# Performance work log

Hardware: AMD Instinct MI355X
Metric: run time of the kernel (lower is better)

The kernel has to match this reference:

```python
import jax, jax.numpy as jnp
import numpy as np

B, S, D, H = 2, 2048, 1024, 16
HD = D // H  # head_dim = 64

def setup_inputs() -> dict:
    key = jax.random.key(0)
    ks = jax.random.split(key, 12)
    sc = 0.02
    return {
        "x": jax.random.normal(ks[0], (B, S, D), dtype=jnp.float32),
        "docking_scores": jax.random.uniform(ks[1], (B, S), dtype=jnp.float32),
        # weights stored as (in, out): y = x @ W + b (equivalent to torch Linear with W=weight.T)
        "Wq": jax.random.normal(ks[2], (D, D), dtype=jnp.float32) * sc,
        "bq": jnp.zeros((D,), dtype=jnp.float32),
        "Wk": jax.random.normal(ks[3], (D, D), dtype=jnp.float32) * sc,
        "bk": jnp.zeros((D,), dtype=jnp.float32),
        "Wv": jax.random.normal(ks[4], (D, D), dtype=jnp.float32) * sc,
        "bv": jnp.zeros((D,), dtype=jnp.float32),
        "Wo": jax.random.normal(ks[5], (D, D), dtype=jnp.float32) * sc,
        "bo": jnp.zeros((D,), dtype=jnp.float32),
        "beta": jnp.asarray(0.5, dtype=jnp.float32),
    }

def reference(x, docking_scores, Wq, bq, Wk, bk, Wv, bv, Wo, bo, beta):
    b, s, d = x.shape
    # project and split heads: (B, H, S, HD)
    def heads(y):
        return y.reshape(b, s, H, HD).transpose(0, 2, 1, 3)
    Q = heads(x @ Wq + bq)
    K = heads(x @ Wk + bk)
    V = heads(x @ Wv + bv)
    # full attention scores (B, H, S, S) — materialized as in the source
    scores = jnp.einsum('bhqd,bhkd->bhqk', Q, K) / np.float32(np.sqrt(HD))
    attn = jax.nn.softmax(scores, axis=-1)
    # docking blend: daa_type != ALL -> blend with per-key docking scores
    ds = docking_scores[:, None, None, :]  # (B, 1, 1, S)
    attn = (1.0 - beta) * attn + beta * ds
    ctx = jnp.einsum('bhqk,bhkd->bhqd', attn, V)
    ctx = ctx.transpose(0, 2, 1, 3).reshape(b, s, d)
    return ctx @ Wo + bo
```

## Files before the change

### kernel.cpp

```cpp
#include <hip/hip_runtime.h>

typedef __attribute__((ext_vector_type(8))) short short8;
typedef __attribute__((ext_vector_type(4))) short short4v;
typedef __attribute__((ext_vector_type(4))) float f32x4;

__device__ __forceinline__ short f2bf(float f) {
  unsigned u = __builtin_bit_cast(unsigned, f);
  u += 0x7fffu + ((u >> 16) & 1u);
  return (short)(u >> 16);
}
__device__ __forceinline__ float bf2f(short s) {
  unsigned u = ((unsigned)(unsigned short)s) << 16;
  return __builtin_bit_cast(float, u);
}
__device__ __forceinline__ void async_load16(const short* g, short* l) {
  __builtin_amdgcn_global_load_lds(
      (const __attribute__((address_space(1))) unsigned int*)g,
      (__attribute__((address_space(3))) unsigned int*)l, 16, 0, 0);
}

__global__ __launch_bounds__(256) void convert_x(const float* __restrict__ x,
                                                 short* __restrict__ xb) {
  int i = (blockIdx.x * 256 + threadIdx.x) * 4;
  float4 v = *(const float4*)(x + i);
  short4v o;
  o[0] = f2bf(v.x); o[1] = f2bf(v.y); o[2] = f2bf(v.z); o[3] = f2bf(v.w);
  *(short4v*)(xb + i) = o;
}

__global__ __launch_bounds__(256) void transpose_w(
    const float* __restrict__ W0, const float* __restrict__ W1,
    const float* __restrict__ W2, const float* __restrict__ W3,
    short* __restrict__ T0, short* __restrict__ T1,
    short* __restrict__ T2, short* __restrict__ T3) {
  const float* W; short* T;
  switch (blockIdx.z) {
    case 0: W = W0; T = T0; break;
    case 1: W = W1; T = T1; break;
    case 2: W = W2; T = T2; break;
    default: W = W3; T = T3; break;
  }
  __shared__ float tile[32][33];
  int tx = threadIdx.x & 31, ty = threadIdx.x >> 5;
  int c = blockIdx.x * 32 + tx;
  #pragma unroll
  for (int i = 0; i < 4; ++i) {
    int r = blockIdx.y * 32 + ty + i * 8;
    tile[ty + i * 8][tx] = W[(size_t)r * 1024 + c];
  }
  __syncthreads();
  int k = blockIdx.y * 32 + tx;
  #pragma unroll
  for (int i = 0; i < 4; ++i) {
    int n = blockIdx.x * 32 + ty + i * 8;
    T[(size_t)n * 1024 + k] = f2bf(tile[tx][ty + i * 8]);
  }
}

__device__ __forceinline__ void gemm_core_128(
    const short* __restrict__ A, const short* __restrict__ Bt,
    int m0, int n0, short* As, short* Bs, f32x4 acc[4][4]) {
  const int tid = threadIdx.x;
  const int wave = tid >> 6, lane = tid & 63;
  const int wm = wave >> 1, wn = wave & 1;
  const int lr = lane & 15, quad = lane >> 4;
  for (int k0 = 0; k0 < 1024; k0 += 32) {
    __syncthreads();
    #pragma unroll
    for (int c2 = 0; c2 < 2; ++c2) {
      int c = wave * 2 + c2;
      int row = c * 16 + (lane >> 2);
      int cbp = lane & 3;
      int sw = (cbp ^ ((row >> 1) & 3)) << 3;
      async_load16(A + (size_t)(m0 + row) * 1024 + k0 + sw, As + c * 512);
      async_load16(Bt + (size_t)(n0 + row) * 1024 + k0 + sw, Bs + c * 512);
    }
    __syncthreads();
    short8 af[4], bf[4];
    #pragma unroll
    for (int i = 0; i < 4; ++i) {
      int ra = wm * 64 + i * 16 + lr;
      af[i] = *(const short8*)(As + ra * 32 + ((quad ^ ((ra >> 1) & 3)) << 3));
      int rb = wn * 64 + i * 16 + lr;
      bf[i] = *(const short8*)(Bs + rb * 32 + ((quad ^ ((rb >> 1) & 3)) << 3));
    }
    #pragma unroll
    for (int i = 0; i < 4; ++i)
      #pragma unroll
      for (int j = 0; j < 4; ++j)
        acc[i][j] = __builtin_amdgcn_mfma_f32_16x16x32_bf16(af[i], bf[j], acc[i][j], 0, 0, 0);
  }
}

__global__ __launch_bounds__(256, 2) void qkv_gemm(
    const short* __restrict__ xb,
    const short* __restrict__ WqT, const short* __restrict__ WkT, const short* __restrict__ WvT,
    const float* __restrict__ bq, const float* __restrict__ bk, const float* __restrict__ bv,
    short* __restrict__ Qb, short* __restrict__ Kb, short* __restrict__ Vt) {
  __shared__ short As[128 * 32];
  __shared__ short Bs[128 * 32];
  int which = blockIdx.x >> 3;
  int n0 = (blockIdx.x & 7) * 128;
  int m0 = blockIdx.y * 128;
  const short* Bt = (which == 0) ? WqT : (which == 1) ? WkT : WvT;
  const float* bias = (which == 0) ? bq : (which == 1) ? bk : bv;
  f32x4 acc[4][4] = {};
  gemm_core_128(xb, Bt, m0, n0, As, Bs, acc);
  const int lane = threadIdx.x & 63, wave = threadIdx.x >> 6;
  const int wm = wave >> 1, wn = wave & 1;
  const int lr = lane & 15, quad = lane >> 4;
  if (which < 2) {
    short* Out = (which == 0) ? Qb : Kb;
    #pragma unroll
    for (int i = 0; i < 4; ++i)
      #pragma unroll
      for (int j = 0; j < 4; ++j) {
        int col = n0 + wn * 64 + j * 16 + lr;
        float bb = bias[col];
        int rowb = m0 + wm * 64 + i * 16 + quad * 4;
        #pragma unroll
        for (int r = 0; r < 4; ++r)
          Out[(size_t)(rowb + r) * 1024 + col] = f2bf(acc[i][j][r] + bb);
      }
  } else {
    #pragma unroll
    for (int i = 0; i < 4; ++i)
      #pragma unroll
      for (int j = 0; j < 4; ++j) {
        int col = n0 + wn * 64 + j * 16 + lr;
        float bb = bias[col];
        int h = col >> 6, d = col & 63;
        int rowb = m0 + wm * 64 + i * 16 + quad * 4;
        int b = rowb >> 11, s = rowb & 2047;
        short4v pk;
        #pragma unroll
        for (int r = 0; r < 4; ++r) pk[r] = f2bf(acc[i][j][r] + bb);
        *(short4v*)(Vt + ((size_t)(b * 16 + h) * 64 + d) * 2048 + s) = pk;
      }
  }
}

__global__ __launch_bounds__(256) void dsv_kernel(const short* __restrict__ Vt,
                                                  const float* __restrict__ ds,
                                                  float* __restrict__ dsV) {
  int bh = blockIdx.x;
  int b = bh >> 4;
  int tid = threadIdx.x;
  int d = tid >> 2, part = tid & 3;
  const short* vrow = Vt + ((size_t)bh * 64 + d) * 2048 + part * 512;
  const float* dsrow = ds + (size_t)b * 2048 + part * 512;
  float acc = 0.f;
  for (int i = 0; i < 512; i += 8) {
    short8 v = *(const short8*)(vrow + i);
    float4 f0 = *(const float4*)(dsrow + i);
    float4 f1 = *(const float4*)(dsrow + i + 4);
    acc += f0.x * bf2f(v[0]) + f0.y * bf2f(v[1]) + f0.z * bf2f(v[2]) + f0.w * bf2f(v[3]);
    acc += f1.x * bf2f(v[4]) + f1.y * bf2f(v[5]) + f1.z * bf2f(v[6]) + f1.w * bf2f(v[7]);
  }
  acc += __shfl_xor(acc, 1);
  acc += __shfl_xor(acc, 2);
  if (part == 0) dsV[bh * 64 + d] = acc;
}

__global__ __launch_bounds__(256, 2) void attn_kernel(
    const short* __restrict__ Qb, const short* __restrict__ Kb,
    const short* __restrict__ Vt, const float* __restrict__ dsV,
    const float* __restrict__ beta_p, short* __restrict__ ctx) {
  __shared__ short Ks[64 * 64];
  __shared__ short Vs[64 * 64];
  __shared__ short Pw[4][32 * 72];
  const int tid = threadIdx.x, wave = tid >> 6, lane = tid & 63;
  const int bh = blockIdx.x >> 4, qt = blockIdx.x & 15;
  const int b = bh >> 4, h = bh & 15;
  const size_t bS = (size_t)b * 2048;
  const int q0 = qt * 128 + wave * 32;
  const int lr = lane & 15, quad = lane >> 4;

  short8 qf[2][2];
  #pragma unroll
  for (int m = 0; m < 2; ++m)
    #pragma unroll
    for (int c = 0; c < 2; ++c)
      qf[m][c] = *(const short8*)(Qb + (bS + q0 + m * 16 + lr) * 1024 + h * 64 + c * 32 + quad * 8);

  f32x4 O[2][4] = {};
  float lacc[2][4] = {};
  short* myP = Pw[wave];

  for (int kt = 0; kt < 32; ++kt) {
    int k0 = kt * 64;
    __syncthreads();
    #pragma unroll
    for (int c2 = 0; c2 < 2; ++c2) {
      int c = wave * 2 + c2;
      int rk = c * 8 + (lane >> 3);
      int cbp = lane & 7;
      int sw = ((cbp ^ (rk & 7)) << 3);
      async_load16(Kb + (bS + k0 + rk) * 1024 + h * 64 + sw, Ks + c * 512);
      async_load16(Vt + ((size_t)bh * 64 + rk) * 2048 + k0 + sw, Vs + c * 512);
    }
    __syncthreads();

    #pragma unroll
    for (int n = 0; n < 4; ++n) {
      int krow = n * 16 + lr;
      short8 kf0 = *(const short8*)(Ks + krow * 64 + ((quad ^ (krow & 7)) << 3));
      short8 kf1 = *(const short8*)(Ks + krow * 64 + (((4 + quad) ^ (krow & 7)) << 3));
      #pragma unroll
      for (int m = 0; m < 2; ++m) {
        f32x4 s = {0.f, 0.f, 0.f, 0.f};
        s = __builtin_amdgcn_mfma_f32_16x16x32_bf16(qf[m][0], kf0, s, 0, 0, 0);
        s = __builtin_amdgcn_mfma_f32_16x16x32_bf16(qf[m][1], kf1, s, 0, 0, 0);
        #pragma unroll
        for (int r = 0; r < 4; ++r) {
          float p = __expf(s[r] * 0.125f);
          lacc[m][r] += p;
          myP[(m * 16 + quad * 4 + r) * 72 + n * 16 + lr] = f2bf(p);
        }
      }
    }
    #pragma unroll
    for (int kc = 0; kc < 2; ++kc) {
      short8 pa[2];
      #pragma unroll
      for (int m = 0; m < 2; ++m)
        pa[m] = *(const short8*)(myP + (m * 16 + lr) * 72 + kc * 32 + quad * 8);
      #pragma unroll
      for (int d = 0; d < 4; ++d) {
        int drow = d * 16 + lr;
        short8 vf = *(const short8*)(Vs + drow * 64 + (((kc * 4 + quad) ^ (drow & 7)) << 3));
        #pragma unroll
        for (int m = 0; m < 2; ++m)
          O[m][d] = __builtin_amdgcn_mfma_f32_16x16x32_bf16(pa[m], vf, O[m][d], 0, 0, 0);
      }
    }
  }

  #pragma unroll
  for (int m = 0; m < 2; ++m)
    #pragma unroll
    for (int r = 0; r < 4; ++r) {
      float v = lacc[m][r];
      v += __shfl_xor(v, 1); v += __shfl_xor(v, 2);
      v += __shfl_xor(v, 4); v += __shfl_xor(v, 8);
      lacc[m][r] = v;
    }
  float beta = *beta_p, omb = 1.f - beta;
  #pragma unroll
  for (int m = 0; m < 2; ++m)
    #pragma unroll
    for (int d = 0; d < 4; ++d) {
      int col = d * 16 + lr;
      float dv = dsV[bh * 64 + col] * beta;
      #pragma unroll
      for (int r = 0; r < 4; ++r) {
        float val = omb * O[m][d][r] / lacc[m][r] + dv;
        size_t row = bS + q0 + m * 16 + quad * 4 + r;
        ctx[row * 1024 + h * 64 + col] = f2bf(val);
      }
    }
}

__global__ __launch_bounds__(256, 2) void out_gemm(
    const short* __restrict__ ctx, const short* __restrict__ WoT,
    const float* __restrict__ bo, float* __restrict__ out) {
  __shared__ short As[128 * 32];
  __shared__ short Bs[128 * 32];
  int n0 = blockIdx.x * 128, m0 = blockIdx.y * 128;
  f32x4 acc[4][4] = {};
  gemm_core_128(ctx, WoT, m0, n0, As, Bs, acc);
  const int lane = threadIdx.x & 63, wave = threadIdx.x >> 6;
  const int wm = wave >> 1, wn = wave & 1;
  const int lr = lane & 15, quad = lane >> 4;
  #pragma unroll
  for (int i = 0; i < 4; ++i)
    #pragma unroll
    for (int j = 0; j < 4; ++j) {
      int col = n0 + wn * 64 + j * 16 + lr;
      float bb = bo[col];
      int rowb = m0 + wm * 64 + i * 16 + quad * 4;
      #pragma unroll
      for (int r = 0; r < 4; ++r)
        out[(size_t)(rowb + r) * 1024 + col] = acc[i][j][r] + bb;
    }
}

extern "C" void kernel_launch(void* const* d_in, const int* in_sizes, int n_in,
                              void* d_out, int out_size, void* d_ws, size_t ws_size,
                              hipStream_t stream) {
  const float* x    = (const float*)d_in[0];
  const float* dsc  = (const float*)d_in[1];
  const float* Wq   = (const float*)d_in[2];
  const float* bq   = (const float*)d_in[3];
  const float* Wk   = (const float*)d_in[4];
  const float* bk   = (const float*)d_in[5];
  const float* Wv   = (const float*)d_in[6];
  const float* bv   = (const float*)d_in[7];
  const float* Wo   = (const float*)d_in[8];
  const float* bo   = (const float*)d_in[9];
  const float* beta = (const float*)d_in[10];

  char* ws = (char*)d_ws;
  const size_t MB = 1u << 20;
  short* xb  = (short*)(ws + 0 * MB);
  short* WqT = (short*)(ws + 8 * MB);
  short* WkT = (short*)(ws + 10 * MB);
  short* WvT = (short*)(ws + 12 * MB);
  short* WoT = (short*)(ws + 14 * MB);
  short* Qb  = (short*)(ws + 16 * MB);
  short* Kb  = (short*)(ws + 24 * MB);
  short* Vt  = (short*)(ws + 32 * MB);
  float* dsV = (float*)(ws + 40 * MB);
  short* ctx = xb;

  convert_x<<<4096, 256, 0, stream>>>(x, xb);
  transpose_w<<<dim3(32, 32, 4), 256, 0, stream>>>(Wq, Wk, Wv, Wo, WqT, WkT, WvT, WoT);
  qkv_gemm<<<dim3(24, 32), 256, 0, stream>>>(xb, WqT, WkT, WvT, bq, bk, bv, Qb, Kb, Vt);
  dsv_kernel<<<32, 256, 0, stream>>>(Vt, dsc, dsV);
  attn_kernel<<<512, 256, 0, stream>>>(Qb, Kb, Vt, dsV, beta, ctx);
  out_gemm<<<dim3(8, 32), 256, 0, stream>>>(ctx, WoT, bo, (float*)d_out);
}
```

Before: 242.3 us.

## Split attention KV range across wave halves, fold softmax scale into Q, retile out GEMM

The attention kernel now runs 512 threads per block. Two wave groups each process half of the key range, and their partial O and row sums are merged through shared memory, which adds parallelism per query tile. The 1/sqrt(d)*log2(e) factor is folded into Q during the QKV GEMM so attention can use a raw exp2 builtin. QK^T is computed transposed and P is packed into a swizzled LDS layout with vector stores. The dsV reduction is split across more blocks using atomics after a memset, and the output GEMM uses 64-row tiles to launch twice as many blocks.

```diff
diff --git a/kernel.cpp b/kernel.cpp
--- a/kernel.cpp
+++ b/kernel.cpp
@@ -3,6 +3,14 @@
 typedef __attribute__((ext_vector_type(8))) short short8;
 typedef __attribute__((ext_vector_type(4))) short short4v;
 typedef __attribute__((ext_vector_type(4))) float f32x4;
+
+#if __has_builtin(__builtin_amdgcn_exp2f)
+#define EXP2F(x) __builtin_amdgcn_exp2f(x)
+#define QSCALE 0.1803368801111601f
+#else
+#define EXP2F(x) __expf(x)
+#define QSCALE 0.125f
+#endif
 
 __device__ __forceinline__ short f2bf(float f) {
   unsigned u = __builtin_bit_cast(unsigned, f);
@@ -76,19 +84,19 @@
       async_load16(Bt + (size_t)(n0 + row) * 1024 + k0 + sw, Bs + c * 512);
     }
     __syncthreads();
-    short8 af[4], bf[4];
+    short8 af[4], bfr[4];
     #pragma unroll
     for (int i = 0; i < 4; ++i) {
       int ra = wm * 64 + i * 16 + lr;
       af[i] = *(const short8*)(As + ra * 32 + ((quad ^ ((ra >> 1) & 3)) << 3));
       int rb = wn * 64 + i * 16 + lr;
-      bf[i] = *(const short8*)(Bs + rb * 32 + ((quad ^ ((rb >> 1) & 3)) << 3));
+      bfr[i] = *(const short8*)(Bs + rb * 32 + ((quad ^ ((rb >> 1) & 3)) << 3));
     }
     #pragma unroll
     for (int i = 0; i < 4; ++i)
       #pragma unroll
       for (int j = 0; j < 4; ++j)
-        acc[i][j] = __builtin_amdgcn_mfma_f32_16x16x32_bf16(af[i], bf[j], acc[i][j], 0, 0, 0);
+        acc[i][j] = __builtin_amdgcn_mfma_f32_16x16x32_bf16(af[i], bfr[j], acc[i][j], 0, 0, 0);
   }
 }
 
@@ -111,6 +119,7 @@
   const int lr = lane & 15, quad = lane >> 4;
   if (which < 2) {
     short* Out = (which == 0) ? Qb : Kb;
+    const float scale = (which == 0) ? QSCALE : 1.0f;
     #pragma unroll
     for (int i = 0; i < 4; ++i)
       #pragma unroll
@@ -120,7 +129,7 @@
         int rowb = m0 + wm * 64 + i * 16 + quad * 4;
         #pragma unroll
         for (int r = 0; r < 4; ++r)
-          Out[(size_t)(rowb + r) * 1024 + col] = f2bf(acc[i][j][r] + bb);
+          Out[(size_t)(rowb + r) * 1024 + col] = f2bf((acc[i][j][r] + bb) * scale);
       }
   } else {
     #pragma unroll
@@ -143,14 +152,14 @@
 __global__ __launch_bounds__(256) void dsv_kernel(const short* __restrict__ Vt,
                                                   const float* __restrict__ ds,
                                                   float* __restrict__ dsV) {
-  int bh = blockIdx.x;
+  int bh = blockIdx.x, sc = blockIdx.y;
   int b = bh >> 4;
-  int tid = threadIdx.x;
-  int d = tid >> 2, part = tid & 3;
-  const short* vrow = Vt + ((size_t)bh * 64 + d) * 2048 + part * 512;
-  const float* dsrow = ds + (size_t)b * 2048 + part * 512;
+  int d = threadIdx.x >> 2, part = threadIdx.x & 3;
+  const short* vrow = Vt + ((size_t)bh * 64 + d) * 2048 + sc * 256 + part * 64;
+  const float* dsrow = ds + (size_t)b * 2048 + sc * 256 + part * 64;
   float acc = 0.f;
-  for (int i = 0; i < 512; i += 8) {
+  #pragma unroll
+  for (int i = 0; i < 64; i += 8) {
     short8 v = *(const short8*)(vrow + i);
     float4 f0 = *(const float4*)(dsrow + i);
     float4 f1 = *(const float4*)(dsrow + i + 4);
@@ -159,126 +168,201 @@
   }
   acc += __shfl_xor(acc, 1);
   acc += __shfl_xor(acc, 2);
-  if (part == 0) dsV[bh * 64 + d] = acc;
-}
-
-__global__ __launch_bounds__(256, 2) void attn_kernel(
+  if (part == 0) atomicAdd(dsV + bh * 64 + d, acc);
+}
+
+__global__ __launch_bounds__(512, 4) void attn_kernel(
     const short* __restrict__ Qb, const short* __restrict__ Kb,
     const short* __restrict__ Vt, const float* __restrict__ dsV,
     const float* __restrict__ beta_p, short* __restrict__ ctx) {
-  __shared__ short Ks[64 * 64];
-  __shared__ short Vs[64 * 64];
-  __shared__ short Pw[4][32 * 72];
+  __shared__ short smem[32768];
   const int tid = threadIdx.x, wave = tid >> 6, lane = tid & 63;
   const int bh = blockIdx.x >> 4, qt = blockIdx.x & 15;
   const int b = bh >> 4, h = bh & 15;
   const size_t bS = (size_t)b * 2048;
-  const int q0 = qt * 128 + wave * 32;
   const int lr = lane & 15, quad = lane >> 4;
+  const int half = wave >> 2;
+  const int qg = wave & 3;
+  const int q0 = qt * 128 + qg * 32;
+
+  short* Ksh = smem + half * 8192;
+  short* Vsh = Ksh + 4096;
+  short* myP = smem + 16384 + wave * 2048;
 
   short8 qf[2][2];
   #pragma unroll
-  for (int m = 0; m < 2; ++m)
+  for (int mb = 0; mb < 2; ++mb)
     #pragma unroll
     for (int c = 0; c < 2; ++c)
-      qf[m][c] = *(const short8*)(Qb + (bS + q0 + m * 16 + lr) * 1024 + h * 64 + c * 32 + quad * 8);
+      qf[mb][c] = *(const short8*)(Qb + (bS + q0 + mb * 16 + lr) * 1024 + h * 64 + c * 32 + quad * 8);
 
   f32x4 O[2][4] = {};
-  float lacc[2][4] = {};
-  short* myP = Pw[wave];
-
-  for (int kt = 0; kt < 32; ++kt) {
-    int k0 = kt * 64;
-    __syncthreads();
-    #pragma unroll
-    for (int c2 = 0; c2 < 2; ++c2) {
-      int c = wave * 2 + c2;
-      int rk = c * 8 + (lane >> 3);
+  float lacc[2] = {0.f, 0.f};
+  const int xs = (lr & 7) << 1;
+
+  for (int t = 0; t < 16; ++t) {
+    const int k0 = (half * 16 + t) * 64;
+    __syncthreads();
+    #pragma unroll
+    for (int c4 = 0; c4 < 4; ++c4) {
+      int c = qg * 4 + c4;
+      int rloc = lane >> 3;
       int cbp = lane & 7;
-      int sw = ((cbp ^ (rk & 7)) << 3);
-      async_load16(Kb + (bS + k0 + rk) * 1024 + h * 64 + sw, Ks + c * 512);
-      async_load16(Vt + ((size_t)bh * 64 + rk) * 2048 + k0 + sw, Vs + c * 512);
-    }
-    __syncthreads();
-
-    #pragma unroll
-    for (int n = 0; n < 4; ++n) {
-      int krow = n * 16 + lr;
-      short8 kf0 = *(const short8*)(Ks + krow * 64 + ((quad ^ (krow & 7)) << 3));
-      short8 kf1 = *(const short8*)(Ks + krow * 64 + (((4 + quad) ^ (krow & 7)) << 3));
-      #pragma unroll
-      for (int m = 0; m < 2; ++m) {
-        f32x4 s = {0.f, 0.f, 0.f, 0.f};
-        s = __builtin_amdgcn_mfma_f32_16x16x32_bf16(qf[m][0], kf0, s, 0, 0, 0);
-        s = __builtin_amdgcn_mfma_f32_16x16x32_bf16(qf[m][1], kf1, s, 0, 0, 0);
+      if (c < 8) {
+        int rk = c * 8 + rloc;
+        int sw = (cbp ^ (rk & 7)) << 3;
+        async_load16(Kb + (bS + k0 + rk) * 1024 + h * 64 + sw, Ksh + c * 512);
+      } else {
+        int cv = c - 8;
+        int rk = cv * 8 + rloc;
+        int sw = (cbp ^ (rk & 7)) << 3;
+        async_load16(Vt + ((size_t)bh * 64 + rk) * 2048 + k0 + sw, Vsh + cv * 512);
+      }
+    }
+    __syncthreads();
+
+    #pragma unroll
+    for (int kb = 0; kb < 4; ++kb) {
+      int krow = kb * 16 + lr;
+      const short* kr = Ksh + krow * 64;
+      short8 kf0 = *(const short8*)(kr + ((quad ^ (krow & 7)) << 3));
+      short8 kf1 = *(const short8*)(kr + (((4 + quad) ^ (krow & 7)) << 3));
+      #pragma unroll
+      for (int mb = 0; mb < 2; ++mb) {
+        f32x4 st = {0.f, 0.f, 0.f, 0.f};
+        st = __builtin_amdgcn_mfma_f32_16x16x32_bf16(kf0, qf[mb][0], st, 0, 0, 0);
+        st = __builtin_amdgcn_mfma_f32_16x16x32_bf16(kf1, qf[mb][1], st, 0, 0, 0);
+        float p0 = EXP2F(st[0]), p1 = EXP2F(st[1]);
+        float p2 = EXP2F(st[2]), p3 = EXP2F(st[3]);
+        lacc[mb] += (p0 + p1) + (p2 + p3);
+        unsigned a0 = __builtin_bit_cast(unsigned, p0) + 0x8000u;
+        unsigned a1 = __builtin_bit_cast(unsigned, p1) + 0x8000u;
+        unsigned a2 = __builtin_bit_cast(unsigned, p2) + 0x8000u;
+        unsigned a3 = __builtin_bit_cast(unsigned, p3) + 0x8000u;
+        uint2 pk;
+        pk.x = (a0 >> 16) | (a1 & 0xffff0000u);
+        pk.y = (a2 >> 16) | (a3 & 0xffff0000u);
+        int qrl = mb * 16 + lr;
+        int phys4 = (kb * 4 + quad) ^ xs;
+        *(uint2*)(myP + qrl * 64 + (phys4 << 2)) = pk;
+      }
+    }
+    #pragma unroll
+    for (int kc = 0; kc < 2; ++kc) {
+      short8 pf[2];
+      #pragma unroll
+      for (int mb = 0; mb < 2; ++mb) {
+        int qrl = mb * 16 + lr;
+        int phys = ((kc * 4 + quad) << 1) ^ xs;
+        pf[mb] = *(const short8*)(myP + qrl * 64 + (phys << 2));
+      }
+      #pragma unroll
+      for (int db = 0; db < 4; ++db) {
+        int drow = db * 16 + lr;
+        short8 vf = *(const short8*)(Vsh + drow * 64 + (((kc * 4 + quad) ^ (drow & 7)) << 3));
         #pragma unroll
-        for (int r = 0; r < 4; ++r) {
-          float p = __expf(s[r] * 0.125f);
-          lacc[m][r] += p;
-          myP[(m * 16 + quad * 4 + r) * 72 + n * 16 + lr] = f2bf(p);
-        }
-      }
-    }
-    #pragma unroll
-    for (int kc = 0; kc < 2; ++kc) {
-      short8 pa[2];
-      #pragma unroll
-      for (int m = 0; m < 2; ++m)
-        pa[m] = *(const short8*)(myP + (m * 16 + lr) * 72 + kc * 32 + quad * 8);
-      #pragma unroll
-      for (int d = 0; d < 4; ++d) {
-        int drow = d * 16 + lr;
-        short8 vf = *(const short8*)(Vs + drow * 64 + (((kc * 4 + quad) ^ (drow & 7)) << 3));
-        #pragma unroll
-        for (int m = 0; m < 2; ++m)
-          O[m][d] = __builtin_amdgcn_mfma_f32_16x16x32_bf16(pa[m], vf, O[m][d], 0, 0, 0);
-      }
-    }
-  }
-
-  #pragma unroll
-  for (int m = 0; m < 2; ++m)
-    #pragma unroll
-    for (int r = 0; r < 4; ++r) {
-      float v = lacc[m][r];
-      v += __shfl_xor(v, 1); v += __shfl_xor(v, 2);
-      v += __shfl_xor(v, 4); v += __shfl_xor(v, 8);
-      lacc[m][r] = v;
-    }
-  float beta = *beta_p, omb = 1.f - beta;
-  #pragma unroll
-  for (int m = 0; m < 2; ++m)
-    #pragma unroll
-    for (int d = 0; d < 4; ++d) {
-      int col = d * 16 + lr;
-      float dv = dsV[bh * 64 + col] * beta;
-      #pragma unroll
-      for (int r = 0; r < 4; ++r) {
-        float val = omb * O[m][d][r] / lacc[m][r] + dv;
-        size_t row = bS + q0 + m * 16 + quad * 4 + r;
-        ctx[row * 1024 + h * 64 + col] = f2bf(val);
-      }
-    }
+        for (int mb = 0; mb < 2; ++mb)
+          O[mb][db] = __builtin_amdgcn_mfma_f32_16x16x32_bf16(vf, pf[mb], O[mb][db], 0, 0, 0);
+      }
+    }
+  }
+
+  float* Obuf = (float*)smem;
+  float* lbuf = (float*)(smem + 16384);
+  __syncthreads();
+  if (half == 1) {
+    #pragma unroll
+    for (int mb = 0; mb < 2; ++mb) {
+      #pragma unroll
+      for (int db = 0; db < 4; ++db)
+        *(f32x4*)(Obuf + ((qg * 2 + mb) * 4 + db) * 256 + lr * 16 + quad * 4) = O[mb][db];
+      lbuf[(qg * 2 + mb) * 64 + quad * 16 + lr] = lacc[mb];
+    }
+  }
+  __syncthreads();
+  if (half == 0) {
+    #pragma unroll
+    for (int mb = 0; mb < 2; ++mb) {
+      #pragma unroll
+      for (int db = 0; db < 4; ++db)
+        O[mb][db] += *(const f32x4*)(Obuf + ((qg * 2 + mb) * 4 + db) * 256 + lr * 16 + quad * 4);
+      lacc[mb] += lbuf[(qg * 2 + mb) * 64 + quad * 16 + lr];
+      float v = lacc[mb];
+      v += __shfl_xor(v, 16);
+      v += __shfl_xor(v, 32);
+      lacc[mb] = v;
+    }
+    float beta = *beta_p;
+    #pragma unroll
+    for (int mb = 0; mb < 2; ++mb) {
+      float linv = (1.f - beta) / lacc[mb];
+      #pragma unroll
+      for (int db = 0; db < 4; ++db) {
+        float4 dv = *(const float4*)(dsV + bh * 64 + db * 16 + quad * 4);
+        short4v o;
+        o[0] = f2bf(O[mb][db][0] * linv + beta * dv.x);
+        o[1] = f2bf(O[mb][db][1] * linv + beta * dv.y);
+        o[2] = f2bf(O[mb][db][2] * linv + beta * dv.z);
+        o[3] = f2bf(O[mb][db][3] * linv + beta * dv.w);
+        *(short4v*)(ctx + (bS + q0 + mb * 16 + lr) * 1024 + h * 64 + db * 16 + quad * 4) = o;
+      }
+    }
+  }
 }
 
 __global__ __launch_bounds__(256, 2) void out_gemm(
     const short* __restrict__ ctx, const short* __restrict__ WoT,
     const float* __restrict__ bo, float* __restrict__ out) {
-  __shared__ short As[128 * 32];
+  __shared__ short As[64 * 32];
   __shared__ short Bs[128 * 32];
-  int n0 = blockIdx.x * 128, m0 = blockIdx.y * 128;
-  f32x4 acc[4][4] = {};
-  gemm_core_128(ctx, WoT, m0, n0, As, Bs, acc);
-  const int lane = threadIdx.x & 63, wave = threadIdx.x >> 6;
+  const int n0 = blockIdx.x * 128, m0 = blockIdx.y * 64;
+  const int tid = threadIdx.x, wave = tid >> 6, lane = tid & 63;
   const int wm = wave >> 1, wn = wave & 1;
   const int lr = lane & 15, quad = lane >> 4;
+  f32x4 acc[2][4] = {};
+  for (int k0 = 0; k0 < 1024; k0 += 32) {
+    __syncthreads();
+    #pragma unroll
+    for (int c3 = 0; c3 < 3; ++c3) {
+      int idx = wave * 3 + c3;
+      int rloc = lane >> 2;
+      int cbp = lane & 3;
+      if (idx < 4) {
+        int row = idx * 16 + rloc;
+        int sw = (cbp ^ ((row >> 1) & 3)) << 3;
+        async_load16(ctx + (size_t)(m0 + row) * 1024 + k0 + sw, As + idx * 512);
+      } else {
+        int c = idx - 4;
+        int row = c * 16 + rloc;
+        int sw = (cbp ^ ((row >> 1) & 3)) << 3;
+        async_load16(WoT + (size_t)(n0 + row) * 1024 + k0 + sw, Bs + c * 512);
+      }
+    }
+    __syncthreads();
+    short8 af[2], bfr[4];
+    #pragma unroll
+    for (int i = 0; i < 2; ++i) {
+      int ra = wm * 32 + i * 16 + lr;
+      af[i] = *(const short8*)(As + ra * 32 + ((quad ^ ((ra >> 1) & 3)) << 3));
+    }
+    #pragma unroll
+    for (int j = 0; j < 4; ++j) {
+      int rb = wn * 64 + j * 16 + lr;
+      bfr[j] = *(const short8*)(Bs + rb * 32 + ((quad ^ ((rb >> 1) & 3)) << 3));
+    }
+    #pragma unroll
+    for (int i = 0; i < 2; ++i)
+      #pragma unroll
+      for (int j = 0; j < 4; ++j)
+        acc[i][j] = __builtin_amdgcn_mfma_f32_16x16x32_bf16(af[i], bfr[j], acc[i][j], 0, 0, 0);
+  }
   #pragma unroll
-  for (int i = 0; i < 4; ++i)
+  for (int i = 0; i < 2; ++i)
     #pragma unroll
     for (int j = 0; j < 4; ++j) {
       int col = n0 + wn * 64 + j * 16 + lr;
       float bb = bo[col];
-      int rowb = m0 + wm * 64 + i * 16 + quad * 4;
+      int rowb = m0 + wm * 32 + i * 16 + quad * 4;
       #pragma unroll
       for (int r = 0; r < 4; ++r)
         out[(size_t)(rowb + r) * 1024 + col] = acc[i][j][r] + bb;
@@ -316,7 +400,8 @@
   convert_x<<<4096, 256, 0, stream>>>(x, xb);
   transpose_w<<<dim3(32, 32, 4), 256, 0, stream>>>(Wq, Wk, Wv, Wo, WqT, WkT, WvT, WoT);
   qkv_gemm<<<dim3(24, 32), 256, 0, stream>>>(xb, WqT, WkT, WvT, bq, bk, bv, Qb, Kb, Vt);
-  dsv_kernel<<<32, 256, 0, stream>>>(Vt, dsc, dsV);
-  attn_kernel<<<512, 256, 0, stream>>>(Qb, Kb, Vt, dsV, beta, ctx);
-  out_gemm<<<dim3(8, 32), 256, 0, stream>>>(ctx, WoT, bo, (float*)d_out);
-}
+  hipMemsetAsync(dsV, 0, 32 * 64 * sizeof(float), stream);
+  dsv_kernel<<<dim3(32, 8), 256, 0, stream>>>(Vt, dsc, dsV);
+  attn_kernel<<<512, 512, 0, stream>>>(Qb, Kb, Vt, dsV, beta, ctx);
+  out_gemm<<<dim3(8, 64), 256, 0, stream>>>(ctx, WoT, bo, (float*)d_out);
+}
```

Measured after the change: 213.0 us. 1.14x faster.
